# Performance work log

Hardware: AMD Instinct MI355X
Metric: run time of the kernel (lower is better)

## Reference

```python
import jax, jax.numpy as jnp
import numpy as np

MARGIN = 1.0
EPS = 1e-10


def setup_inputs() -> dict:
    key = jax.random.key(0)
    k1, k2, k3 = jax.random.split(key, 3)
    C, D = 4096, 1024
    B, A = 8, 32
    cls_features = jax.random.normal(k1, (C, D), dtype=jnp.float32)
    prototypes = jax.random.normal(k2, (C, D), dtype=jnp.float32)
    annotations = jax.random.randint(k3, (B, A, 5), 0, C, dtype=jnp.int64)
    return {"cls_features": cls_features, "prototypes": prototypes,
            "annotations": annotations, "steps": 1000}


def reference(cls_features, prototypes, annotations, steps):
    C, D = cls_features.shape
    protos = jax.lax.stop_gradient(prototypes)  # prototypes.detach()

    # one_hot presence of each class in the batch annotations (col 4 = class id, -1 = pad)
    targets = annotations[:, :, 4]                      # [B, A]
    valid = targets != -1
    counts = jnp.zeros((C,), jnp.float32).at[
        jnp.where(valid, targets, 0).ravel()
    ].add(valid.astype(jnp.float32).ravel())
    mask_i = counts > 0                                  # class present in batch
    mask_j = jnp.sum(protos, axis=-1) != 0               # prototypes[j].sum() != 0

    # pairwise mean squared distance: msd[i, j] = mean((feat_i - proto_j)^2)
    f2 = jnp.sum(cls_features * cls_features, axis=-1)   # [C]
    p2 = jnp.sum(protos * protos, axis=-1)               # [C]
    cross = cls_features @ protos.T                      # [C, C]
    msd = jnp.maximum(f2[:, None] + p2[None, :] - 2.0 * cross, 0.0) / D

    pair_mask = mask_i[:, None] & mask_j[None, :]
    eye = jnp.eye(C, dtype=bool)
    intra_mask = pair_mask & eye
    inter_mask = pair_mask & ~eye

    intra_count = jnp.sum(intra_mask.astype(jnp.float32))
    inter_count = jnp.sum(inter_mask.astype(jnp.float32))

    intra_loss = jnp.sum(jnp.where(intra_mask, msd, 0.0)) / (intra_count + EPS)

    s = jnp.sqrt(jnp.maximum(msd, 1e-12))
    e = MARGIN - s
    inter_term = (e / MARGIN) ** 2 * jnp.maximum(e, 0.0) ** 2
    inter_loss = jnp.sum(jnp.where(inter_mask, inter_term, 0.0)) / (inter_count + EPS)

    return (intra_loss, inter_loss)
```

## Files before the change

### kernel.cpp

```cpp
#include <hip/hip_runtime.h>
#include <hip/hip_bf16.h>

typedef float f32x4 __attribute__((ext_vector_type(4)));
typedef int   i32x4 __attribute__((ext_vector_type(4)));
typedef int   i32x8 __attribute__((ext_vector_type(8)));

#define NC 4096
#define ND 1024
#define NVP 256
#define EPSF 1e-10f
#define SCALE1 127


__global__ __launch_bounds__(256)
void fprep_kernel(const int* __restrict__ ann, int n_ann,
                  const float* __restrict__ F,
                  unsigned char* __restrict__ Fc, float* __restrict__ f2c,
                  int* __restrict__ vidx, int* __restrict__ nv,
                  float* __restrict__ accum) {
  __shared__ unsigned char mark[NC];
  __shared__ int wsum[4];
  __shared__ int vloc[NVP];
  __shared__ float rs[4];
  const int tid = threadIdx.x;
  const int lane = tid & 63, wid = tid >> 6;

  for (int i = tid; i < NC; i += 256) mark[i] = 0;
  __syncthreads();
  for (int t = tid; t < n_ann; t += 256) {
    int idx = ann[t * 5 + 4];
    if (idx >= 0 && idx < NC) mark[idx] = 1;
  }
  __syncthreads();
  int base = tid * 16, lc = 0;
  #pragma unroll
  for (int k = 0; k < 16; ++k) lc += mark[base + k];
  int inc = lc;
  #pragma unroll
  for (int off = 1; off < 64; off <<= 1) {
    int v = __shfl_up(inc, off);
    if (lane >= off) inc += v;
  }
  if (lane == 63) wsum[wid] = inc;
  __syncthreads();
  int wbase = 0;
  for (int w = 0; w < wid; ++w) wbase += wsum[w];
  int pos = wbase + inc - lc;
  for (int k = 0; k < 16; ++k)
    if (mark[base + k]) vloc[pos++] = base + k;
  const int total = wsum[0] + wsum[1] + wsum[2] + wsum[3];
  __syncthreads();

  if (blockIdx.x == 0) {
    for (int i = tid; i < NVP; i += 256) vidx[i] = (i < total) ? vloc[i] : 0;
    if (tid == 0) *nv = total;
    if (tid < 8) accum[tid] = 0.f;
  }

  const int slot = blockIdx.x;
  if (slot >= total) return;

  const int row = vloc[slot];
  float4 v = *reinterpret_cast<const float4*>(F + (size_t)row * ND + tid * 4);
  int pk = __builtin_amdgcn_cvt_pk_fp8_f32(v.x, v.y, 0, false);
  pk = __builtin_amdgcn_cvt_pk_fp8_f32(v.z, v.w, pk, true);
  {
    int d0 = tid * 4;
    int kt = d0 >> 7, hif = (d0 >> 5) & 3, half = (d0 >> 4) & 1, b = d0 & 15;
    int R16 = slot >> 4, lof = slot & 15;
    size_t fa = ((((size_t)kt * 16 + R16) * 2 + half) * 64 + hif * 16 + lof) * 16 + b;
    *reinterpret_cast<int*>(Fc + fa) = pk;
  }
  float sq = v.x * v.x + v.y * v.y + v.z * v.z + v.w * v.w;
  #pragma unroll
  for (int off = 32; off; off >>= 1) sq += __shfl_down(sq, off);
  if (lane == 0) rs[wid] = sq;
  __syncthreads();
  if (tid == 0) f2c[slot] = rs[0] + rs[1] + rs[2] + rs[3];
}

#define LDFRAG(V, BASEPTR, FID)                                               \
  do {                                                                        \
    const unsigned char* _p = (BASEPTR) + (size_t)(FID) * 2048 + lane * 16;   \
    i32x4 _l0 = *(const i32x4*)(_p);                                          \
    i32x4 _l1 = *(const i32x4*)(_p + 1024);                                   \
    V = __builtin_shufflevector(_l0, _l1, 0, 1, 2, 3, 4, 5, 6, 7);            \
  } while (0)

__global__ __launch_bounds__(512)
void pgemm_kernel(const float* __restrict__ P,
                  const unsigned char* __restrict__ Fc,
                  const float* __restrict__ f2c,
                  const int* __restrict__ vidx, const int* __restrict__ nv,
                  float* __restrict__ psum, float* __restrict__ accum) {
  __shared__ __attribute__((aligned(16))) unsigned char bfrag[8 * 2048];
  __shared__ float p2l[16], psl[16], redI[8], redE[8];
  const int tid = threadIdx.x;
  const int lane = tid & 63, wid = tid >> 6;
  const int bj = blockIdx.x;

  {
    const int r = tid >> 5;
    const int seg = tid & 31;
    const float* src = P + (size_t)(bj * 16 + r) * ND;
    float sq = 0.f, sm = 0.f;
    #pragma unroll
    for (int i = 0; i < 8; ++i) {
      float4 v = *reinterpret_cast<const float4*>(src + (seg + i * 32) * 4);
      int pk = __builtin_amdgcn_cvt_pk_fp8_f32(v.x, v.y, 0, false);
      pk = __builtin_amdgcn_cvt_pk_fp8_f32(v.z, v.w, pk, true);
      int addr = i * 2048 + r * 128 + ((seg * 4) ^ ((r & 7) << 4));
      *reinterpret_cast<int*>(&bfrag[addr]) = pk;
      sq += v.x * v.x + v.y * v.y + v.z * v.z + v.w * v.w;
      sm += v.x + v.y + v.z + v.w;
    }
    #pragma unroll
    for (int off = 16; off; off >>= 1) {
      sq += __shfl_down(sq, off, 32);
      sm += __shfl_down(sm, off, 32);
    }
    if ((tid & 31) == 0) {
      p2l[r] = sq; psl[r] = sm;
      psum[bj * 16 + r] = sm;
    }
  }
  __syncthreads();

  const int lo = lane & 15, hi = lane >> 4;
  f32x4 acc0 = {0.f, 0.f, 0.f, 0.f}, acc1 = acc0;
  const int fbase = wid * 2;
  #pragma unroll 4
  for (int kt = 0; kt < 8; ++kt) {
    i32x8 a0, a1, b;
    LDFRAG(a0, Fc, kt * 16 + fbase);
    LDFRAG(a1, Fc, kt * 16 + fbase + 1);
    {
      int x = (lo & 7) << 4;
      const unsigned char* bb = &bfrag[kt * 2048 + lo * 128];
      i32x4 l0 = *reinterpret_cast<const i32x4*>(bb + ((hi * 32) ^ x));
      i32x4 l1 = *reinterpret_cast<const i32x4*>(bb + ((hi * 32 + 16) ^ x));
      b = __builtin_shufflevector(l0, l1, 0, 1, 2, 3, 4, 5, 6, 7);
    }
    acc0 = __builtin_amdgcn_mfma_scale_f32_16x16x128_f8f6f4(
        a0, b, acc0, 0, 0, 0, SCALE1, 0, SCALE1);
    acc1 = __builtin_amdgcn_mfma_scale_f32_16x16x128_f8f6f4(
        a1, b, acc1, 0, 0, 0, SCALE1, 0, SCALE1);
  }

  int Nv = *nv;
  float intra_l = 0.f, inter_l = 0.f;
  const int gj = bj * 16 + lo;
  const float p2j = p2l[lo];
  const bool mj = psl[lo] != 0.f;
  if (mj) {
    #pragma unroll
    for (int f = 0; f < 2; ++f) {
      f32x4 a = f ? acc1 : acc0;
      #pragma unroll
      for (int r = 0; r < 4; ++r) {
        int ci = wid * 32 + f * 16 + hi * 4 + r;
        if (ci < Nv) {
          float msd = fmaxf(f2c[ci] + p2j - 2.f * a[r], 0.f) * (1.f / 1024.f);
          int gi = vidx[ci];
          if (gi == gj) {
            intra_l += msd;
          } else if (msd < 1.0f) {
            float s = sqrtf(fmaxf(msd, 1e-12f));
            float e = 1.f - s;
            float e2 = e * e;
            inter_l += e2 * e2;
          }
        }
      }
    }
  }
  #pragma unroll
  for (int off = 32; off; off >>= 1) {
    intra_l += __shfl_down(intra_l, off);
    inter_l += __shfl_down(inter_l, off);
  }
  if (lane == 0) { redI[wid] = intra_l; redE[wid] = inter_l; }
  __syncthreads();
  if (tid == 0) {
    float si = 0.f, se = 0.f;
    #pragma unroll
    for (int w = 0; w < 8; ++w) { si += redI[w]; se += redE[w]; }
    atomicAdd(&accum[0], si);
    atomicAdd(&accum[1], se);
  }
}

__global__ void finalize_kernel(const float* __restrict__ psum,
                                const int* __restrict__ vidx,
                                const int* __restrict__ nv,
                                const float* __restrict__ accum,
                                float* __restrict__ out) {
  __shared__ int r1[4], r2[4];
  int tid = threadIdx.x;
  int Nv = *nv;
  int nj = 0, nd = 0;
  for (int i = tid; i < NC; i += 256) nj += (psum[i] != 0.f);
  for (int c = tid; c < Nv; c += 256) nd += (psum[vidx[c]] != 0.f);
  #pragma unroll
  for (int off = 32; off; off >>= 1) {
    nj += __shfl_down(nj, off);
    nd += __shfl_down(nd, off);
  }
  int wid = tid >> 6, lane = tid & 63;
  if (lane == 0) { r1[wid] = nj; r2[wid] = nd; }
  __syncthreads();
  if (tid == 0) {
    float fni = (float)Nv;
    float fnj = (float)(r1[0] + r1[1] + r1[2] + r1[3]);
    float fnd = (float)(r2[0] + r2[1] + r2[2] + r2[3]);
    out[0] = accum[0] / (fnd + EPSF);
    out[1] = accum[1] / (fni * fnj - fnd + EPSF);
  }
}

extern "C" void kernel_launch(void* const* d_in, const int* in_sizes, int n_in,
                              void* d_out, int out_size, void* d_ws, size_t ws_size,
                              hipStream_t stream) {
  const float* F = (const float*)d_in[0];
  const float* P = (const float*)d_in[1];
  const int* ann = (const int*)d_in[2];
  int n_ann = in_sizes[2] / 5;

  char* ws = (char*)d_ws;
  unsigned char* Fc = (unsigned char*)ws;
  float* f2c   = (float*)(ws + (size_t)NVP * ND);
  float* psum  = f2c + NVP;
  float* accum = psum + NC;
  int*   vidx  = (int*)(accum + 8);
  int*   nv    = vidx + NVP;

  float* out = (float*)d_out;

  fprep_kernel<<<NVP, 256, 0, stream>>>(ann, n_ann, F, Fc, f2c, vidx, nv, accum);
  pgemm_kernel<<<NC / 16, 512, 0, stream>>>(P, Fc, f2c, vidx, nv, psum, accum);
  finalize_kernel<<<1, 256, 0, stream>>>(psum, vidx, nv, accum, out);
}
```

Measured before the change: 28.56 us.

## Fuse finalize into GEMM kernel via last-block ticket and recompute class list per block

Result: slower. 42.71 us (+49.6%).

```diff
diff --git a/kernel.cpp b/kernel.cpp
--- a/kernel.cpp
+++ b/kernel.cpp
@@ -16,8 +16,7 @@
 void fprep_kernel(const int* __restrict__ ann, int n_ann,
                   const float* __restrict__ F,
                   unsigned char* __restrict__ Fc, float* __restrict__ f2c,
-                  int* __restrict__ vidx, int* __restrict__ nv,
-                  float* __restrict__ accum) {
+                  float* __restrict__ accum, int* __restrict__ ticket) {
   __shared__ unsigned char mark[NC];
   __shared__ int wsum[4];
   __shared__ int vloc[NVP];
@@ -52,14 +51,12 @@
   __syncthreads();
 
   if (blockIdx.x == 0) {
-    for (int i = tid; i < NVP; i += 256) vidx[i] = (i < total) ? vloc[i] : 0;
-    if (tid == 0) *nv = total;
     if (tid < 8) accum[tid] = 0.f;
+    if (tid == 8) *ticket = 0;
   }
 
   const int slot = blockIdx.x;
   if (slot >= total) return;
-
   const int row = vloc[slot];
   float4 v = *reinterpret_cast<const float4*>(F + (size_t)row * ND + tid * 4);
   int pk = __builtin_amdgcn_cvt_pk_fp8_f32(v.x, v.y, 0, false);
@@ -76,7 +73,7 @@
   for (int off = 32; off; off >>= 1) sq += __shfl_down(sq, off);
   if (lane == 0) rs[wid] = sq;
   __syncthreads();
-  if (tid == 0) f2c[slot] = rs[0] + rs[1] + rs[2] + rs[3];
+  if (tid == 0) f2c[slot] = sq = rs[0] + rs[1] + rs[2] + rs[3];
 }
 
 #define LDFRAG(V, BASEPTR, FID)                                               \
@@ -88,16 +85,54 @@
   } while (0)
 
 __global__ __launch_bounds__(512)
-void pgemm_kernel(const float* __restrict__ P,
+void pgemm_kernel(const int* __restrict__ ann, int n_ann,
+                  const float* __restrict__ P,
                   const unsigned char* __restrict__ Fc,
                   const float* __restrict__ f2c,
-                  const int* __restrict__ vidx, const int* __restrict__ nv,
-                  float* __restrict__ psum, float* __restrict__ accum) {
+                  float* __restrict__ accum, int* __restrict__ ticket,
+                  float* __restrict__ out) {
+  __shared__ unsigned char mark[NC];
+  __shared__ int vloc[NVP];
+  __shared__ int wsum[8];
   __shared__ __attribute__((aligned(16))) unsigned char bfrag[8 * 2048];
   __shared__ float p2l[16], psl[16], redI[8], redE[8];
+  __shared__ int tkt;
   const int tid = threadIdx.x;
   const int lane = tid & 63, wid = tid >> 6;
   const int bj = blockIdx.x;
+
+  for (int i = tid; i < NC; i += 512) mark[i] = 0;
+  __syncthreads();
+  for (int t = tid; t < n_ann; t += 512) {
+    int idx = ann[t * 5 + 4];
+    if (idx >= 0 && idx < NC) mark[idx] = 1;
+  }
+  __syncthreads();
+  int lc = 0;
+  {
+    int base = tid * 8;
+    #pragma unroll
+    for (int k = 0; k < 8; ++k) lc += mark[base + k];
+  }
+  int inc = lc;
+  #pragma unroll
+  for (int off = 1; off < 64; off <<= 1) {
+    int v = __shfl_up(inc, off);
+    if (lane >= off) inc += v;
+  }
+  if (lane == 63) wsum[wid] = inc;
+  __syncthreads();
+  int wbase = 0;
+  for (int w = 0; w < wid; ++w) wbase += wsum[w];
+  int pos = wbase + inc - lc;
+  {
+    int base = tid * 8;
+    for (int k = 0; k < 8; ++k)
+      if (mark[base + k]) vloc[pos++] = base + k;
+  }
+  const int total = wsum[0] + wsum[1] + wsum[2] + wsum[3] +
+                    wsum[4] + wsum[5] + wsum[6] + wsum[7];
+  __syncthreads();
 
   {
     const int r = tid >> 5;
@@ -119,10 +154,7 @@
       sq += __shfl_down(sq, off, 32);
       sm += __shfl_down(sm, off, 32);
     }
-    if ((tid & 31) == 0) {
-      p2l[r] = sq; psl[r] = sm;
-      psum[bj * 16 + r] = sm;
-    }
+    if ((tid & 31) == 0) { p2l[r] = sq; psl[r] = sm; }
   }
   __syncthreads();
 
@@ -147,28 +179,29 @@
         a1, b, acc1, 0, 0, 0, SCALE1, 0, SCALE1);
   }
 
-  int Nv = *nv;
   float intra_l = 0.f, inter_l = 0.f;
-  const int gj = bj * 16 + lo;
-  const float p2j = p2l[lo];
-  const bool mj = psl[lo] != 0.f;
-  if (mj) {
-    #pragma unroll
-    for (int f = 0; f < 2; ++f) {
-      f32x4 a = f ? acc1 : acc0;
+  {
+    const int gj = bj * 16 + lo;
+    const float p2j = p2l[lo];
+    const bool mj = psl[lo] != 0.f;
+    if (mj) {
       #pragma unroll
-      for (int r = 0; r < 4; ++r) {
-        int ci = wid * 32 + f * 16 + hi * 4 + r;
-        if (ci < Nv) {
-          float msd = fmaxf(f2c[ci] + p2j - 2.f * a[r], 0.f) * (1.f / 1024.f);
-          int gi = vidx[ci];
-          if (gi == gj) {
-            intra_l += msd;
-          } else if (msd < 1.0f) {
-            float s = sqrtf(fmaxf(msd, 1e-12f));
-            float e = 1.f - s;
-            float e2 = e * e;
-            inter_l += e2 * e2;
+      for (int f = 0; f < 2; ++f) {
+        f32x4 a = f ? acc1 : acc0;
+        #pragma unroll
+        for (int r = 0; r < 4; ++r) {
+          int ci = wid * 32 + f * 16 + hi * 4 + r;
+          if (ci < total) {
+            float msd = fmaxf(f2c[ci] + p2j - 2.f * a[r], 0.f) * (1.f / 1024.f);
+            int gi = vloc[ci];
+            if (gi == gj) {
+              intra_l += msd;
+            } else if (msd < 1.0f) {
+              float s = sqrtf(fmaxf(msd, 1e-12f));
+              float e = 1.f - s;
+              float e2 = e * e;
+              inter_l += e2 * e2;
+            }
           }
         }
       }
@@ -181,40 +214,35 @@
   }
   if (lane == 0) { redI[wid] = intra_l; redE[wid] = inter_l; }
   __syncthreads();
+
   if (tid == 0) {
     float si = 0.f, se = 0.f;
     #pragma unroll
     for (int w = 0; w < 8; ++w) { si += redI[w]; se += redE[w]; }
     atomicAdd(&accum[0], si);
     atomicAdd(&accum[1], se);
-  }
-}
-
-__global__ void finalize_kernel(const float* __restrict__ psum,
-                                const int* __restrict__ vidx,
-                                const int* __restrict__ nv,
-                                const float* __restrict__ accum,
-                                float* __restrict__ out) {
-  __shared__ int r1[4], r2[4];
-  int tid = threadIdx.x;
-  int Nv = *nv;
-  int nj = 0, nd = 0;
-  for (int i = tid; i < NC; i += 256) nj += (psum[i] != 0.f);
-  for (int c = tid; c < Nv; c += 256) nd += (psum[vidx[c]] != 0.f);
-  #pragma unroll
-  for (int off = 32; off; off >>= 1) {
-    nj += __shfl_down(nj, off);
-    nd += __shfl_down(nd, off);
-  }
-  int wid = tid >> 6, lane = tid & 63;
-  if (lane == 0) { r1[wid] = nj; r2[wid] = nd; }
-  __syncthreads();
-  if (tid == 0) {
-    float fni = (float)Nv;
-    float fnj = (float)(r1[0] + r1[1] + r1[2] + r1[3]);
-    float fnd = (float)(r2[0] + r2[1] + r2[2] + r2[3]);
-    out[0] = accum[0] / (fnd + EPSF);
-    out[1] = accum[1] / (fni * fnj - fnd + EPSF);
+    int nj = 0, nd = 0;
+    #pragma unroll
+    for (int r = 0; r < 16; ++r) nj += (psl[r] != 0.f);
+    for (int c = 0; c < total; ++c) {
+      int v = vloc[c];
+      if ((v >> 4) == bj && psl[v & 15] != 0.f) ++nd;
+    }
+    atomicAdd(&accum[2], (float)nj);
+    atomicAdd(&accum[3], (float)nd);
+    __threadfence();
+    tkt = atomicAdd(ticket, 1);
+  }
+  __syncthreads();
+
+  if (tkt == (NC / 16) - 1 && tid == 0) {
+    float a0 = atomicAdd(&accum[0], 0.f);
+    float a1 = atomicAdd(&accum[1], 0.f);
+    float nj = atomicAdd(&accum[2], 0.f);
+    float nd = atomicAdd(&accum[3], 0.f);
+    float ni = (float)total;
+    out[0] = a0 / (nd + EPSF);
+    out[1] = a1 / (ni * nj - nd + EPSF);
   }
 }
 
@@ -228,15 +256,12 @@
 
   char* ws = (char*)d_ws;
   unsigned char* Fc = (unsigned char*)ws;
-  float* f2c   = (float*)(ws + (size_t)NVP * ND);
-  float* psum  = f2c + NVP;
-  float* accum = psum + NC;
-  int*   vidx  = (int*)(accum + 8);
-  int*   nv    = vidx + NVP;
+  float* f2c    = (float*)(ws + (size_t)NVP * ND);
+  float* accum  = f2c + NVP;
+  int*   ticket = (int*)(accum + 8);
 
   float* out = (float*)d_out;
 
-  fprep_kernel<<<NVP, 256, 0, stream>>>(ann, n_ann, F, Fc, f2c, vidx, nv, accum);
-  pgemm_kernel<<<NC / 16, 512, 0, stream>>>(P, Fc, f2c, vidx, nv, psum, accum);
-  finalize_kernel<<<1, 256, 0, stream>>>(psum, vidx, nv, accum, out);
+  fprep_kernel<<<NVP, 256, 0, stream>>>(ann, n_ann, F, Fc, f2c, accum, ticket);
+  pgemm_kernel<<<NC / 16, 512, 0, stream>>>(ann, n_ann, P, Fc, f2c, accum, ticket, out);
 }
```
